# Optimization experiments

Measured on AMD Instinct MI355X. Metric: run time of the kernel, lower is better.

The kernel has to match this reference:

```python
import jax, jax.numpy as jnp
import numpy as np

N_NODES = 100000
N_EDGES = 1600000
N_FEAT = 512
N_HID = 256
N_CLASS = 40


def setup_inputs() -> dict:
    key = jax.random.key(0)
    ks = jax.random.split(key, 6)
    features = jax.random.normal(ks[0], (N_NODES, N_FEAT), dtype=jnp.float32)
    edge_index = jax.random.randint(ks[1], (2, N_EDGES), 0, N_NODES, dtype=jnp.int32)
    edge_weight = jax.random.uniform(ks[2], (N_EDGES,), dtype=jnp.float32)
    # xavier_uniform with gain=1.414 (as in reset_parameters)
    g = 1.414
    lim1 = g * np.sqrt(6.0 / (N_FEAT + N_HID))
    lim2 = g * np.sqrt(6.0 / (N_HID + N_CLASS))
    W1 = jax.random.uniform(ks[3], (N_FEAT, N_HID), minval=-lim1, maxval=lim1, dtype=jnp.float32)
    W2 = jax.random.uniform(ks[4], (N_HID, N_CLASS), minval=-lim2, maxval=lim2, dtype=jnp.float32)
    b1 = jnp.zeros((N_HID,), dtype=jnp.float32)
    b2 = jnp.zeros((N_CLASS,), dtype=jnp.float32)
    return {"features": features, "edge_index": edge_index, "edge_weight": edge_weight,
            "W1": W1, "b1": b1, "W2": W2, "b2": b2}


def _spmm(edge_index, edge_weight, x, n):
    # out[r] = sum over edges e with row[e]==r of w[e] * x[col[e]]
    row, col = edge_index[0], edge_index[1]
    msgs = edge_weight[:, None] * x[col]  # [E, D]
    return jax.ops.segment_sum(msgs, row, num_segments=n)


def reference(features, edge_index, edge_weight, W1, b1, W2, b2):
    n = features.shape[0]
    # Layer 1: linear -> spmm -> relu (dropout is identity in eval mode)
    h = features @ W1 + b1
    h = jax.nn.relu(_spmm(edge_index, edge_weight, h, n))
    # Layer 2: linear -> spmm -> log_softmax
    h = h @ W2 + b2
    h = _spmm(edge_index, edge_weight, h, n)
    return jax.nn.log_softmax(h, axis=1)
```

## Files before the change

### kernel.cpp

```cpp
#include <hip/hip_runtime.h>
#include <stdint.h>

#define N_NODES 100000
#define N_EDGES 1600000
#define N_FEAT 512
#define N_HID 256
#define N_CLASS 40
#define H2S 48

typedef float f32x4 __attribute__((ext_vector_type(4)));
typedef __bf16 bf16x8 __attribute__((ext_vector_type(8)));
typedef unsigned short u16x4 __attribute__((ext_vector_type(4)));
typedef unsigned short u16x8 __attribute__((ext_vector_type(8)));

__device__ __forceinline__ unsigned short f2bf(float f) {
  unsigned int u = __float_as_uint(f);
  unsigned int r = (u + 0x7FFFu + ((u >> 16) & 1u)) >> 16;
  return (unsigned short)r;
}
__device__ __forceinline__ float bf2f(unsigned short s) {
  return __uint_as_float(((unsigned int)s) << 16);
}

__device__ __forceinline__ void gll16(const void* g, void* l) {
  __builtin_amdgcn_global_load_lds(
      (const __attribute__((address_space(1))) unsigned int*)g,
      (__attribute__((address_space(3))) unsigned int*)l, 16, 0, 0);
}

#define HIST_BLOCKS 1563
#define W1T_BLOCKS  512
#define W2T_BLOCKS  48
__global__ __launch_bounds__(256) void k_pre(const float* __restrict__ W1,
                                             const float* __restrict__ W2,
                                             const int* __restrict__ ei,
                                             unsigned short* __restrict__ W1t,
                                             unsigned short* __restrict__ W2t,
                                             int* __restrict__ cnt,
                                             int* __restrict__ rank) {
  const int bid = blockIdx.x, tid = threadIdx.x;
  if (bid < HIST_BLOCKS) {
    #pragma unroll
    for (int k = 0; k < 4; ++k) {
      int e = bid * 1024 + k * 256 + tid;
      if (e < N_EDGES) rank[e] = atomicAdd(&cnt[ei[e]], 1);
    }
  } else if (bid < HIST_BLOCKS + W1T_BLOCKS) {
    int gid = (bid - HIST_BLOCKS) * 256 + tid;
    int n = gid >> 9, k = gid & 511;
    W1t[gid] = f2bf(W1[(long)k * N_HID + n]);
  } else {
    int gid = (bid - HIST_BLOCKS - W1T_BLOCKS) * 256 + tid;
    int n = gid >> 8, k = gid & 255;
    W2t[gid] = (n < N_CLASS) ? f2bf(W2[(long)k * N_CLASS + n]) : (unsigned short)0;
  }
}

__global__ __launch_bounds__(1024) void k_scan_a(const int* __restrict__ cnt,
                                                 int* __restrict__ rp,
                                                 int* __restrict__ bsum) {
  __shared__ int sm[1024];
  const int tid = threadIdx.x;
  const int i = blockIdx.x * 1024 + tid;
  int v = (i < N_NODES) ? cnt[i] : 0;
  sm[tid] = v;
  __syncthreads();
  #pragma unroll
  for (int d = 1; d < 1024; d <<= 1) {
    int t = (tid >= d) ? sm[tid - d] : 0;
    __syncthreads();
    sm[tid] += t;
    __syncthreads();
  }
  if (i < N_NODES) rp[i] = sm[tid] - v;
  if (tid == 1023) bsum[blockIdx.x] = sm[1023];
}

__global__ __launch_bounds__(128) void k_scan_b(const int* __restrict__ bsum,
                                                int* __restrict__ boffs,
                                                int* __restrict__ rp) {
  __shared__ int sm[128];
  const int tid = threadIdx.x;
  const int nb = (N_NODES + 1023) >> 10;
  int v = (tid < nb) ? bsum[tid] : 0;
  sm[tid] = v;
  __syncthreads();
  #pragma unroll
  for (int d = 1; d < 128; d <<= 1) {
    int t = (tid >= d) ? sm[tid - d] : 0;
    __syncthreads();
    sm[tid] += t;
    __syncthreads();
  }
  boffs[tid] = sm[tid] - v;
  if (tid == 127) rp[N_NODES] = sm[127];
}

__global__ void k_scan_c(int* __restrict__ rp, const int* __restrict__ boffs) {
  int i = blockIdx.x * 256 + threadIdx.x;
  if (i >= N_NODES) return;
  rp[i] += boffs[i >> 10];
}

#define NG1 782
__global__ __launch_bounds__(512) void k_fused1(const float* __restrict__ X,
                                                const unsigned short* __restrict__ W1t,
                                                const float* __restrict__ b1,
                                                unsigned short* __restrict__ H1,
                                                const int* __restrict__ ei,
                                                const float* __restrict__ ew,
                                                const int* __restrict__ rank,
                                                const int* __restrict__ rp,
                                                int2* __restrict__ cw) {
  const int t = threadIdx.x;

  if (blockIdx.x & 1) {
    int sb = blockIdx.x >> 1;
    #pragma unroll
    for (int k = 0; k < 4; ++k) {
      int e = sb * 2048 + k * 512 + t;
      if (e < N_EDGES) {
        int r = ei[e];
        int pos = rp[r] + rank[e];
        cw[pos] = make_int2(ei[N_EDGES + e], __float_as_int(ew[e]));
      }
    }
    return;
  }

  __shared__ __align__(16) float As[128 * 32];
  __shared__ __align__(16) unsigned short Bsm[256 * 32];
  const int gb = blockIdx.x >> 1;
  const long m0 = (long)gb * 128;
  const int lane = t & 63;
  const int wid = t >> 6;
  const int wm = wid >> 2, wn = wid & 3;
  const int lr = lane & 15;
  const int lkg = lane >> 4;

  const int a_row = t >> 3, a_ps = t & 7;
  const int b_row = t >> 2, b_ps = t & 3;
  long a_gr0 = m0 + a_row;      if (a_gr0 >= N_NODES) a_gr0 = N_NODES - 1;
  long a_gr1 = m0 + 64 + a_row; if (a_gr1 >= N_NODES) a_gr1 = N_NODES - 1;
  const float* a_src0 = X + a_gr0 * N_FEAT + ((a_ps ^ (a_row & 7)) << 2);
  const float* a_src1 = X + a_gr1 * N_FEAT + ((a_ps ^ (a_row & 7)) << 2);
  const unsigned short* b_src0 = W1t + (long)b_row * N_FEAT + ((b_ps ^ ((b_row >> 2) & 3)) << 3);
  const unsigned short* b_src1 = W1t + (long)(128 + b_row) * N_FEAT + ((b_ps ^ ((b_row >> 2) & 3)) << 3);
  char* a_dst = (char*)As + wid * 1024;
  char* b_dst = (char*)Bsm + wid * 1024;

  f32x4 acc[4][4] = {};

  for (int k0 = 0; k0 < N_FEAT; k0 += 32) {
    gll16(a_src0 + k0, a_dst);
    gll16(a_src1 + k0, a_dst + 8192);
    gll16(b_src0 + k0, b_dst);
    gll16(b_src1 + k0, b_dst + 8192);
    __syncthreads();

    bf16x8 bv[4];
    #pragma unroll
    for (int nt = 0; nt < 4; ++nt) {
      int row = wn * 64 + nt * 16 + lr;
      int ps = lkg ^ ((lr >> 2) & 3);
      bv[nt] = *(const bf16x8*)((const char*)Bsm + row * 64 + ps * 16);
    }
    #pragma unroll
    for (int mt = 0; mt < 4; ++mt) {
      int row = wm * 64 + mt * 16 + lr;
      int s0 = (2 * lkg) ^ (lr & 7);
      int s1 = (2 * lkg + 1) ^ (lr & 7);
      f32x4 xa = *(const f32x4*)((const char*)As + row * 128 + s0 * 16);
      f32x4 xb = *(const f32x4*)((const char*)As + row * 128 + s1 * 16);
      bf16x8 av;
      av[0] = (__bf16)xa[0]; av[1] = (__bf16)xa[1];
      av[2] = (__bf16)xa[2]; av[3] = (__bf16)xa[3];
      av[4] = (__bf16)xb[0]; av[5] = (__bf16)xb[1];
      av[6] = (__bf16)xb[2]; av[7] = (__bf16)xb[3];
      #pragma unroll
      for (int nt = 0; nt < 4; ++nt)
        acc[mt][nt] = __builtin_amdgcn_mfma_f32_16x16x32_bf16(av, bv[nt], acc[mt][nt], 0, 0, 0);
    }
    __syncthreads();
  }

  #pragma unroll
  for (int nt = 0; nt < 4; ++nt) {
    int col = wn * 64 + nt * 16 + lr;
    float bias = b1[col];
    #pragma unroll
    for (int mt = 0; mt < 4; ++mt) {
      #pragma unroll
      for (int i = 0; i < 4; ++i) {
        long row = m0 + wm * 64 + mt * 16 + lkg * 4 + i;
        if (row < N_NODES) H1[row * N_HID + col] = f2bf(acc[mt][nt][i] + bias);
      }
    }
  }
}

__global__ __launch_bounds__(256) void k_spmm1(const int* __restrict__ row_ptr,
                                               const int2* __restrict__ cw,
                                               const unsigned short* __restrict__ H1,
                                               unsigned short* __restrict__ H1r) {
  int r = blockIdx.x * 4 + (threadIdx.x >> 6);
  int lane = threadIdx.x & 63;
  if (r >= N_NODES) return;
  int s = row_ptr[r], e = row_ptr[r + 1];
  float a0 = 0.f, a1 = 0.f, a2 = 0.f, a3 = 0.f;
  const unsigned short* Hb = H1 + lane * 4;
  int i = s;
  for (; i + 8 <= e; i += 8) {
    int2 c0 = cw[i + 0]; int2 c1 = cw[i + 1]; int2 c2 = cw[i + 2]; int2 c3 = cw[i + 3];
    int2 c4 = cw[i + 4]; int2 c5 = cw[i + 5]; int2 c6 = cw[i + 6]; int2 c7 = cw[i + 7];
    u16x4 h0 = *(const u16x4*)(Hb + (long)c0.x * N_HID);
    u16x4 h1 = *(const u16x4*)(Hb + (long)c1.x * N_HID);
    u16x4 h2 = *(const u16x4*)(Hb + (long)c2.x * N_HID);
    u16x4 h3 = *(const u16x4*)(Hb + (long)c3.x * N_HID);
    u16x4 h4 = *(const u16x4*)(Hb + (long)c4.x * N_HID);
    u16x4 h5 = *(const u16x4*)(Hb + (long)c5.x * N_HID);
    u16x4 h6 = *(const u16x4*)(Hb + (long)c6.x * N_HID);
    u16x4 h7 = *(const u16x4*)(Hb + (long)c7.x * N_HID);
    float w0 = __int_as_float(c0.y), w1 = __int_as_float(c1.y);
    float w2 = __int_as_float(c2.y), w3 = __int_as_float(c3.y);
    float w4 = __int_as_float(c4.y), w5 = __int_as_float(c5.y);
    float w6 = __int_as_float(c6.y), w7 = __int_as_float(c7.y);
    a0 += w0 * bf2f(h0[0]); a1 += w0 * bf2f(h0[1]); a2 += w0 * bf2f(h0[2]); a3 += w0 * bf2f(h0[3]);
    a0 += w1 * bf2f(h1[0]); a1 += w1 * bf2f(h1[1]); a2 += w1 * bf2f(h1[2]); a3 += w1 * bf2f(h1[3]);
    a0 += w2 * bf2f(h2[0]); a1 += w2 * bf2f(h2[1]); a2 += w2 * bf2f(h2[2]); a3 += w2 * bf2f(h2[3]);
    a0 += w3 * bf2f(h3[0]); a1 += w3 * bf2f(h3[1]); a2 += w3 * bf2f(h3[2]); a3 += w3 * bf2f(h3[3]);
    a0 += w4 * bf2f(h4[0]); a1 += w4 * bf2f(h4[1]); a2 += w4 * bf2f(h4[2]); a3 += w4 * bf2f(h4[3]);
    a0 += w5 * bf2f(h5[0]); a1 += w5 * bf2f(h5[1]); a2 += w5 * bf2f(h5[2]); a3 += w5 * bf2f(h5[3]);
    a0 += w6 * bf2f(h6[0]); a1 += w6 * bf2f(h6[1]); a2 += w6 * bf2f(h6[2]); a3 += w6 * bf2f(h6[3]);
    a0 += w7 * bf2f(h7[0]); a1 += w7 * bf2f(h7[1]); a2 += w7 * bf2f(h7[2]); a3 += w7 * bf2f(h7[3]);
  }
  for (; i < e; ++i) {
    int2 cwv = cw[i];
    float w = __int_as_float(cwv.y);
    u16x4 hv = *(const u16x4*)(Hb + (long)cwv.x * N_HID);
    a0 += w * bf2f(hv[0]);
    a1 += w * bf2f(hv[1]);
    a2 += w * bf2f(hv[2]);
    a3 += w * bf2f(hv[3]);
  }
  u16x4 o;
  o[0] = f2bf(fmaxf(a0, 0.f));
  o[1] = f2bf(fmaxf(a1, 0.f));
  o[2] = f2bf(fmaxf(a2, 0.f));
  o[3] = f2bf(fmaxf(a3, 0.f));
  *(u16x4*)(H1r + (long)r * N_HID + lane * 4) = o;
}

__global__ __launch_bounds__(256) void k_gemm2(const unsigned short* __restrict__ H1r,
                                               const unsigned short* __restrict__ W2t,
                                               const float* __restrict__ b2,
                                               float* __restrict__ H2) {
  const int t = threadIdx.x;
  const int lane = t & 63;
  const int wid = t >> 6;
  const long m0 = (long)blockIdx.x * 128;
  const int lr = lane & 15;
  const int lk = (lane >> 4) * 8;

  const unsigned short* Ab[2];
  #pragma unroll
  for (int mt = 0; mt < 2; ++mt) {
    long r = m0 + wid * 32 + mt * 16 + lr;
    if (r >= N_NODES) r = N_NODES - 1;
    Ab[mt] = H1r + r * N_HID + lk;
  }
  const unsigned short* Bb[3];
  #pragma unroll
  for (int nt = 0; nt < 3; ++nt)
    Bb[nt] = W2t + (long)(nt * 16 + lr) * N_HID + lk;

  f32x4 acc[2][3] = {};
  #pragma unroll
  for (int k0 = 0; k0 < N_HID; k0 += 32) {
    bf16x8 av[2], bvv[3];
    #pragma unroll
    for (int mt = 0; mt < 2; ++mt) av[mt] = *(const bf16x8*)(Ab[mt] + k0);
    #pragma unroll
    for (int nt = 0; nt < 3; ++nt) bvv[nt] = *(const bf16x8*)(Bb[nt] + k0);
    #pragma unroll
    for (int mt = 0; mt < 2; ++mt)
      #pragma unroll
      for (int nt = 0; nt < 3; ++nt)
        acc[mt][nt] = __builtin_amdgcn_mfma_f32_16x16x32_bf16(av[mt], bvv[nt], acc[mt][nt], 0, 0, 0);
  }

  #pragma unroll
  for (int nt = 0; nt < 3; ++nt) {
    int col = nt * 16 + lr;
    if (col < N_CLASS) {
      float bias = b2[col];
      #pragma unroll
      for (int mt = 0; mt < 2; ++mt) {
        #pragma unroll
        for (int i = 0; i < 4; ++i) {
          long row = m0 + wid * 32 + mt * 16 + (lane >> 4) * 4 + i;
          if (row < N_NODES) H2[row * H2S + col] = acc[mt][nt][i] + bias;
        }
      }
    }
  }
}

__global__ __launch_bounds__(256) void k_spmm2_lsm(const int* __restrict__ row_ptr,
                                                   const int2* __restrict__ cw,
                                                   const float* __restrict__ H2,
                                                   float* __restrict__ out) {
  int r = blockIdx.x * 4 + (threadIdx.x >> 6);
  int lane = threadIdx.x & 63;
  if (r >= N_NODES) return;
  int s = row_ptr[r], e = row_ptr[r + 1];
  float acc = 0.f;
  const bool act = lane < N_CLASS;
  int i = s;
  for (; i + 8 <= e; i += 8) {
    int2 c0 = cw[i + 0]; int2 c1 = cw[i + 1]; int2 c2 = cw[i + 2]; int2 c3 = cw[i + 3];
    int2 c4 = cw[i + 4]; int2 c5 = cw[i + 5]; int2 c6 = cw[i + 6]; int2 c7 = cw[i + 7];
    float h0 = 0.f, h1 = 0.f, h2 = 0.f, h3 = 0.f, h4 = 0.f, h5 = 0.f, h6 = 0.f, h7 = 0.f;
    if (act) {
      h0 = H2[(long)c0.x * H2S + lane];
      h1 = H2[(long)c1.x * H2S + lane];
      h2 = H2[(long)c2.x * H2S + lane];
      h3 = H2[(long)c3.x * H2S + lane];
      h4 = H2[(long)c4.x * H2S + lane];
      h5 = H2[(long)c5.x * H2S + lane];
      h6 = H2[(long)c6.x * H2S + lane];
      h7 = H2[(long)c7.x * H2S + lane];
    }
    acc += __int_as_float(c0.y) * h0;
    acc += __int_as_float(c1.y) * h1;
    acc += __int_as_float(c2.y) * h2;
    acc += __int_as_float(c3.y) * h3;
    acc += __int_as_float(c4.y) * h4;
    acc += __int_as_float(c5.y) * h5;
    acc += __int_as_float(c6.y) * h6;
    acc += __int_as_float(c7.y) * h7;
  }
  for (; i < e; ++i) {
    int2 cwv = cw[i];
    if (act) acc += __int_as_float(cwv.y) * H2[(long)cwv.x * H2S + lane];
  }
  float v = act ? acc : -INFINITY;
  float m = v;
  #pragma unroll
  for (int d = 32; d > 0; d >>= 1) m = fmaxf(m, __shfl_xor(m, d));
  float ex = act ? __expf(v - m) : 0.f;
  float ssum = ex;
  #pragma unroll
  for (int d = 32; d > 0; d >>= 1) ssum += __shfl_xor(ssum, d);
  float ls = __logf(ssum);
  if (act) out[(long)r * N_CLASS + lane] = v - m - ls;
}

extern "C" void kernel_launch(void* const* d_in, const int* in_sizes, int n_in,
                              void* d_out, int out_size, void* d_ws, size_t ws_size,
                              hipStream_t stream) {
  (void)in_sizes; (void)n_in; (void)out_size; (void)ws_size;
  const float* X  = (const float*)d_in[0];
  const int*   EI = (const int*)d_in[1];
  const float* EW = (const float*)d_in[2];
  const float* W1 = (const float*)d_in[3];
  const float* b1 = (const float*)d_in[4];
  const float* W2 = (const float*)d_in[5];
  const float* b2 = (const float*)d_in[6];
  float* out = (float*)d_out;

  char* p = (char*)d_ws;
  auto take = [&](size_t bytes) {
    char* r = p;
    p += (bytes + 511) & ~(size_t)511;
    return r;
  };
  unsigned short* W1t   = (unsigned short*)take((size_t)N_HID * N_FEAT * 2);
  unsigned short* W2t   = (unsigned short*)take((size_t)48 * N_HID * 2);
  int*            cnt   = (int*)take((size_t)N_NODES * 4);
  int*            rp    = (int*)take((size_t)(N_NODES + 1) * 4);
  int*            bsum  = (int*)take((size_t)128 * 4);
  int*            boffs = (int*)take((size_t)128 * 4);
  int*            rank  = (int*)take((size_t)N_EDGES * 4);
  int2*           cw    = (int2*)take((size_t)N_EDGES * 8);
  unsigned short* H1    = (unsigned short*)take((size_t)N_NODES * N_HID * 2);
  unsigned short* H1r   = (unsigned short*)take((size_t)N_NODES * N_HID * 2);
  float*          H2    = (float*)take((size_t)N_NODES * H2S * 4);

  const int NB_SCAN = (N_NODES + 1023) / 1024;

  hipMemsetAsync(cnt, 0, (size_t)N_NODES * 4, stream);
  k_pre<<<HIST_BLOCKS + W1T_BLOCKS + W2T_BLOCKS, 256, 0, stream>>>(W1, W2, EI, W1t, W2t, cnt, rank);
  k_scan_a<<<NB_SCAN, 1024, 0, stream>>>(cnt, rp, bsum);
  k_scan_b<<<1, 128, 0, stream>>>(bsum, boffs, rp);
  k_scan_c<<<(N_NODES + 255) / 256, 256, 0, stream>>>(rp, boffs);
  k_fused1<<<2 * NG1, 512, 0, stream>>>(X, W1t, b1, H1, EI, EW, rank, rp, cw);
  k_spmm1<<<(N_NODES + 3) / 4, 256, 0, stream>>>(rp, cw, H1, H1r);
  k_gemm2<<<(N_NODES + 127) / 128, 256, 0, stream>>>(H1r, W2t, b2, H2);
  k_spmm2_lsm<<<(N_NODES + 3) / 4, 256, 0, stream>>>(rp, cw, H2, out);
}
```

Measured before the change: 461.4 us.

## Pack CSR column and bf16 weight into one word; restructure GEMM1 with resident W1 panel

Edge entries are packed into a single 32-bit word (17-bit column index, 15-bit truncated bf16 weight), halving CSR traffic in both SpMM passes and allowing uint4 vector loads. The fused GEMM+scatter kernel is split into a separate scatter kernel and a new GEMM1 that keeps a 128-column W1 panel entirely in LDS (128 KB), with each wave streaming X rows directly from global memory rather than staging them through LDS. This removes the per-k-step barriers, but it sacrifices the overlap between the scatter and the GEMM, reduces edge-weight precision to 15 bits, and limits the GEMM to 250 blocks.

Result: faster. 427.0 us (-7.5%).

```diff
diff --git a/kernel.cpp b/kernel.cpp
--- a/kernel.cpp
+++ b/kernel.cpp
@@ -21,12 +21,10 @@
 __device__ __forceinline__ float bf2f(unsigned short s) {
   return __uint_as_float(((unsigned int)s) << 16);
 }
-
-__device__ __forceinline__ void gll16(const void* g, void* l) {
-  __builtin_amdgcn_global_load_lds(
-      (const __attribute__((address_space(1))) unsigned int*)g,
-      (__attribute__((address_space(3))) unsigned int*)l, 16, 0, 0);
-}
+__device__ __forceinline__ float pk_w(unsigned int p) {
+  return __uint_as_float((p >> 17) << 16);
+}
+__device__ __forceinline__ int pk_c(unsigned int p) { return (int)(p & 0x1FFFFu); }
 
 #define HIST_BLOCKS 1563
 #define W1T_BLOCKS  512
@@ -102,105 +100,89 @@
   rp[i] += boffs[i >> 10];
 }
 
-#define NG1 782
-__global__ __launch_bounds__(512) void k_fused1(const float* __restrict__ X,
+__global__ __launch_bounds__(512) void k_scatter(const int* __restrict__ ei,
+                                                 const float* __restrict__ ew,
+                                                 const int* __restrict__ rank,
+                                                 const int* __restrict__ rp,
+                                                 unsigned int* __restrict__ cwp) {
+  const int t = threadIdx.x;
+  #pragma unroll
+  for (int k = 0; k < 4; ++k) {
+    int e = blockIdx.x * 2048 + k * 512 + t;
+    if (e < N_EDGES) {
+      int r = ei[e];
+      int pos = rp[r] + rank[e];
+      unsigned int w15 = (unsigned int)f2bf(ew[e]);
+      cwp[pos] = (w15 << 17) | (unsigned int)ei[N_EDGES + e];
+    }
+  }
+}
+
+__global__ __launch_bounds__(1024) void k_gemm1(const float* __restrict__ X,
                                                 const unsigned short* __restrict__ W1t,
                                                 const float* __restrict__ b1,
-                                                unsigned short* __restrict__ H1,
-                                                const int* __restrict__ ei,
-                                                const float* __restrict__ ew,
-                                                const int* __restrict__ rank,
-                                                const int* __restrict__ rp,
-                                                int2* __restrict__ cw) {
+                                                unsigned short* __restrict__ H1) {
+  __shared__ __align__(16) unsigned short Bs[128 * 512];
   const int t = threadIdx.x;
-
-  if (blockIdx.x & 1) {
-    int sb = blockIdx.x >> 1;
-    #pragma unroll
-    for (int k = 0; k < 4; ++k) {
-      int e = sb * 2048 + k * 512 + t;
-      if (e < N_EDGES) {
-        int r = ei[e];
-        int pos = rp[r] + rank[e];
-        cw[pos] = make_int2(ei[N_EDGES + e], __float_as_int(ew[e]));
-      }
-    }
-    return;
-  }
-
-  __shared__ __align__(16) float As[128 * 32];
-  __shared__ __align__(16) unsigned short Bsm[256 * 32];
-  const int gb = blockIdx.x >> 1;
-  const long m0 = (long)gb * 128;
+  const int pair = blockIdx.x >> 1, panel = blockIdx.x & 1;
+  const long rb = (long)pair * 800;
+  const int n0 = panel * 128;
+
+  {
+    const int col = t >> 3, seg = t & 7;
+    const unsigned short* src = W1t + (long)(n0 + col) * N_FEAT;
+    #pragma unroll
+    for (int j = 0; j < 8; ++j) {
+      int slot = seg * 8 + j;
+      int ps = slot ^ (col & 7);
+      *(u16x8*)&Bs[col * 512 + ps * 8] = *(const u16x8*)(src + slot * 8);
+    }
+  }
+  __syncthreads();
+
   const int lane = t & 63;
   const int wid = t >> 6;
-  const int wm = wid >> 2, wn = wid & 3;
   const int lr = lane & 15;
   const int lkg = lane >> 4;
 
-  const int a_row = t >> 3, a_ps = t & 7;
-  const int b_row = t >> 2, b_ps = t & 3;
-  long a_gr0 = m0 + a_row;      if (a_gr0 >= N_NODES) a_gr0 = N_NODES - 1;
-  long a_gr1 = m0 + 64 + a_row; if (a_gr1 >= N_NODES) a_gr1 = N_NODES - 1;
-  const float* a_src0 = X + a_gr0 * N_FEAT + ((a_ps ^ (a_row & 7)) << 2);
-  const float* a_src1 = X + a_gr1 * N_FEAT + ((a_ps ^ (a_row & 7)) << 2);
-  const unsigned short* b_src0 = W1t + (long)b_row * N_FEAT + ((b_ps ^ ((b_row >> 2) & 3)) << 3);
-  const unsigned short* b_src1 = W1t + (long)(128 + b_row) * N_FEAT + ((b_ps ^ ((b_row >> 2) & 3)) << 3);
-  char* a_dst = (char*)As + wid * 1024;
-  char* b_dst = (char*)Bsm + wid * 1024;
-
-  f32x4 acc[4][4] = {};
-
-  for (int k0 = 0; k0 < N_FEAT; k0 += 32) {
-    gll16(a_src0 + k0, a_dst);
-    gll16(a_src1 + k0, a_dst + 8192);
-    gll16(b_src0 + k0, b_dst);
-    gll16(b_src1 + k0, b_dst + 8192);
-    __syncthreads();
-
-    bf16x8 bv[4];
-    #pragma unroll
-    for (int nt = 0; nt < 4; ++nt) {
-      int row = wn * 64 + nt * 16 + lr;
-      int ps = lkg ^ ((lr >> 2) & 3);
-      bv[nt] = *(const bf16x8*)((const char*)Bsm + row * 64 + ps * 16);
-    }
-    #pragma unroll
-    for (int mt = 0; mt < 4; ++mt) {
-      int row = wm * 64 + mt * 16 + lr;
-      int s0 = (2 * lkg) ^ (lr & 7);
-      int s1 = (2 * lkg + 1) ^ (lr & 7);
-      f32x4 xa = *(const f32x4*)((const char*)As + row * 128 + s0 * 16);
-      f32x4 xb = *(const f32x4*)((const char*)As + row * 128 + s1 * 16);
+  for (int c = wid; c < 50; c += 16) {
+    const long row0 = rb + c * 16;
+    const float* ap = X + (row0 + lr) * N_FEAT + lkg * 8;
+    f32x4 acc[8] = {};
+
+    #pragma unroll 2
+    for (int k0 = 0; k0 < N_FEAT; k0 += 32) {
+      f32x4 xa = *(const f32x4*)(ap + k0);
+      f32x4 xb = *(const f32x4*)(ap + k0 + 4);
       bf16x8 av;
       av[0] = (__bf16)xa[0]; av[1] = (__bf16)xa[1];
       av[2] = (__bf16)xa[2]; av[3] = (__bf16)xa[3];
       av[4] = (__bf16)xb[0]; av[5] = (__bf16)xb[1];
       av[6] = (__bf16)xb[2]; av[7] = (__bf16)xb[3];
+      const int slot = (k0 >> 3) + lkg;
+      const int ps = slot ^ (lr & 7);
       #pragma unroll
-      for (int nt = 0; nt < 4; ++nt)
-        acc[mt][nt] = __builtin_amdgcn_mfma_f32_16x16x32_bf16(av, bv[nt], acc[mt][nt], 0, 0, 0);
-    }
-    __syncthreads();
-  }
-
-  #pragma unroll
-  for (int nt = 0; nt < 4; ++nt) {
-    int col = wn * 64 + nt * 16 + lr;
-    float bias = b1[col];
-    #pragma unroll
-    for (int mt = 0; mt < 4; ++mt) {
+      for (int nt = 0; nt < 8; ++nt) {
+        bf16x8 bv = *(const bf16x8*)&Bs[(nt * 16 + lr) * 512 + ps * 8];
+        acc[nt] = __builtin_amdgcn_mfma_f32_16x16x32_bf16(av, bv, acc[nt], 0, 0, 0);
+      }
+    }
+
+    #pragma unroll
+    for (int nt = 0; nt < 8; ++nt) {
+      int colg = n0 + nt * 16 + lr;
+      float bias = b1[colg];
       #pragma unroll
       for (int i = 0; i < 4; ++i) {
-        long row = m0 + wm * 64 + mt * 16 + lkg * 4 + i;
-        if (row < N_NODES) H1[row * N_HID + col] = f2bf(acc[mt][nt][i] + bias);
+        long row = row0 + lkg * 4 + i;
+        H1[row * N_HID + colg] = f2bf(acc[nt][i] + bias);
       }
     }
   }
 }
 
 __global__ __launch_bounds__(256) void k_spmm1(const int* __restrict__ row_ptr,
-                                               const int2* __restrict__ cw,
+                                               const unsigned int* __restrict__ cwp,
                                                const unsigned short* __restrict__ H1,
                                                unsigned short* __restrict__ H1r) {
   int r = blockIdx.x * 4 + (threadIdx.x >> 6);
@@ -211,20 +193,18 @@
   const unsigned short* Hb = H1 + lane * 4;
   int i = s;
   for (; i + 8 <= e; i += 8) {
-    int2 c0 = cw[i + 0]; int2 c1 = cw[i + 1]; int2 c2 = cw[i + 2]; int2 c3 = cw[i + 3];
-    int2 c4 = cw[i + 4]; int2 c5 = cw[i + 5]; int2 c6 = cw[i + 6]; int2 c7 = cw[i + 7];
-    u16x4 h0 = *(const u16x4*)(Hb + (long)c0.x * N_HID);
-    u16x4 h1 = *(const u16x4*)(Hb + (long)c1.x * N_HID);
-    u16x4 h2 = *(const u16x4*)(Hb + (long)c2.x * N_HID);
-    u16x4 h3 = *(const u16x4*)(Hb + (long)c3.x * N_HID);
-    u16x4 h4 = *(const u16x4*)(Hb + (long)c4.x * N_HID);
-    u16x4 h5 = *(const u16x4*)(Hb + (long)c5.x * N_HID);
-    u16x4 h6 = *(const u16x4*)(Hb + (long)c6.x * N_HID);
-    u16x4 h7 = *(const u16x4*)(Hb + (long)c7.x * N_HID);
-    float w0 = __int_as_float(c0.y), w1 = __int_as_float(c1.y);
-    float w2 = __int_as_float(c2.y), w3 = __int_as_float(c3.y);
-    float w4 = __int_as_float(c4.y), w5 = __int_as_float(c5.y);
-    float w6 = __int_as_float(c6.y), w7 = __int_as_float(c7.y);
+    uint4 ca = *(const uint4*)(cwp + i);
+    uint4 cb = *(const uint4*)(cwp + i + 4);
+    u16x4 h0 = *(const u16x4*)(Hb + (long)pk_c(ca.x) * N_HID);
+    u16x4 h1 = *(const u16x4*)(Hb + (long)pk_c(ca.y) * N_HID);
+    u16x4 h2 = *(const u16x4*)(Hb + (long)pk_c(ca.z) * N_HID);
+    u16x4 h3 = *(const u16x4*)(Hb + (long)pk_c(ca.w) * N_HID);
+    u16x4 h4 = *(const u16x4*)(Hb + (long)pk_c(cb.x) * N_HID);
+    u16x4 h5 = *(const u16x4*)(Hb + (long)pk_c(cb.y) * N_HID);
+    u16x4 h6 = *(const u16x4*)(Hb + (long)pk_c(cb.z) * N_HID);
+    u16x4 h7 = *(const u16x4*)(Hb + (long)pk_c(cb.w) * N_HID);
+    float w0 = pk_w(ca.x), w1 = pk_w(ca.y), w2 = pk_w(ca.z), w3 = pk_w(ca.w);
+    float w4 = pk_w(cb.x), w5 = pk_w(cb.y), w6 = pk_w(cb.z), w7 = pk_w(cb.w);
     a0 += w0 * bf2f(h0[0]); a1 += w0 * bf2f(h0[1]); a2 += w0 * bf2f(h0[2]); a3 += w0 * bf2f(h0[3]);
     a0 += w1 * bf2f(h1[0]); a1 += w1 * bf2f(h1[1]); a2 += w1 * bf2f(h1[2]); a3 += w1 * bf2f(h1[3]);
     a0 += w2 * bf2f(h2[0]); a1 += w2 * bf2f(h2[1]); a2 += w2 * bf2f(h2[2]); a3 += w2 * bf2f(h2[3]);
@@ -235,9 +215,9 @@
     a0 += w7 * bf2f(h7[0]); a1 += w7 * bf2f(h7[1]); a2 += w7 * bf2f(h7[2]); a3 += w7 * bf2f(h7[3]);
   }
   for (; i < e; ++i) {
-    int2 cwv = cw[i];
-    float w = __int_as_float(cwv.y);
-    u16x4 hv = *(const u16x4*)(Hb + (long)cwv.x * N_HID);
+    unsigned int p = cwp[i];
+    float w = pk_w(p);
+    u16x4 hv = *(const u16x4*)(Hb + (long)pk_c(p) * N_HID);
     a0 += w * bf2f(hv[0]);
     a1 += w * bf2f(hv[1]);
     a2 += w * bf2f(hv[2]);
@@ -307,7 +287,7 @@
 }
 
 __global__ __launch_bounds__(256) void k_spmm2_lsm(const int* __restrict__ row_ptr,
-                                                   const int2* __restrict__ cw,
+                                                   const unsigned int* __restrict__ cwp,
                                                    const float* __restrict__ H2,
                                                    float* __restrict__ out) {
   int r = blockIdx.x * 4 + (threadIdx.x >> 6);
@@ -318,31 +298,31 @@
   const bool act = lane < N_CLASS;
   int i = s;
   for (; i + 8 <= e; i += 8) {
-    int2 c0 = cw[i + 0]; int2 c1 = cw[i + 1]; int2 c2 = cw[i + 2]; int2 c3 = cw[i + 3];
-    int2 c4 = cw[i + 4]; int2 c5 = cw[i + 5]; int2 c6 = cw[i + 6]; int2 c7 = cw[i + 7];
+    uint4 ca = *(const uint4*)(cwp + i);
+    uint4 cb = *(const uint4*)(cwp + i + 4);
     float h0 = 0.f, h1 = 0.f, h2 = 0.f, h3 = 0.f, h4 = 0.f, h5 = 0.f, h6 = 0.f, h7 = 0.f;
     if (act) {
-      h0 = H2[(long)c0.x * H2S + lane];
-      h1 = H2[(long)c1.x * H2S + lane];
-      h2 = H2[(long)c2.x * H2S + lane];
-      h3 = H2[(long)c3.x * H2S + lane];
-      h4 = H2[(long)c4.x * H2S + lane];
-      h5 = H2[(long)c5.x * H2S + lane];
-      h6 = H2[(long)c6.x * H2S + lane];
-      h7 = H2[(long)c7.x * H2S + lane];
-    }
-    acc += __int_as_float(c0.y) * h0;
-    acc += __int_as_float(c1.y) * h1;
-    acc += __int_as_float(c2.y) * h2;
-    acc += __int_as_float(c3.y) * h3;
-    acc += __int_as_float(c4.y) * h4;
-    acc += __int_as_float(c5.y) * h5;
-    acc += __int_as_float(c6.y) * h6;
-    acc += __int_as_float(c7.y) * h7;
+      h0 = H2[(long)pk_c(ca.x) * H2S + lane];
+      h1 = H2[(long)pk_c(ca.y) * H2S + lane];
+      h2 = H2[(long)pk_c(ca.z) * H2S + lane];
+      h3 = H2[(long)pk_c(ca.w) * H2S + lane];
+      h4 = H2[(long)pk_c(cb.x) * H2S + lane];
+      h5 = H2[(long)pk_c(cb.y) * H2S + lane];
+      h6 = H2[(long)pk_c(cb.z) * H2S + lane];
+      h7 = H2[(long)pk_c(cb.w) * H2S + lane];
+    }
+    acc += pk_w(ca.x) * h0;
+    acc += pk_w(ca.y) * h1;
+    acc += pk_w(ca.z) * h2;
+    acc += pk_w(ca.w) * h3;
+    acc += pk_w(cb.x) * h4;
+    acc += pk_w(cb.y) * h5;
+    acc += pk_w(cb.z) * h6;
+    acc += pk_w(cb.w) * h7;
   }
   for (; i < e; ++i) {
-    int2 cwv = cw[i];
-    if (act) acc += __int_as_float(cwv.y) * H2[(long)cwv.x * H2S + lane];
+    unsigned int p = cwp[i];
+    if (act) acc += pk_w(p) * H2[(long)pk_c(p) * H2S + lane];
   }
   float v = act ? acc : -INFINITY;
   float m = v;
@@ -382,7 +362,7 @@
   int*            bsum  = (int*)take((size_t)128 * 4);
   int*            boffs = (int*)take((size_t)128 * 4);
   int*            rank  = (int*)take((size_t)N_EDGES * 4);
-  int2*           cw    = (int2*)take((size_t)N_EDGES * 8);
+  unsigned int*   cwp   = (unsigned int*)take((size_t)N_EDGES * 4);
   unsigned short* H1    = (unsigned short*)take((size_t)N_NODES * N_HID * 2);
   unsigned short* H1r   = (unsigned short*)take((size_t)N_NODES * N_HID * 2);
   float*          H2    = (float*)take((size_t)N_NODES * H2S * 4);
@@ -394,8 +374,9 @@
   k_scan_a<<<NB_SCAN, 1024, 0, stream>>>(cnt, rp, bsum);
   k_scan_b<<<1, 128, 0, stream>>>(bsum, boffs, rp);
   k_scan_c<<<(N_NODES + 255) / 256, 256, 0, stream>>>(rp, boffs);
-  k_fused1<<<2 * NG1, 512, 0, stream>>>(X, W1t, b1, H1, EI, EW, rank, rp, cw);
-  k_spmm1<<<(N_NODES + 3) / 4, 256, 0, stream>>>(rp, cw, H1, H1r);
+  k_scatter<<<(N_EDGES + 2047) / 2048, 512, 0, stream>>>(EI, EW, rank, rp, cwp);
+  k_gemm1<<<250, 1024, 0, stream>>>(X, W1t, b1, H1);
+  k_spmm1<<<(N_NODES + 3) / 4, 256, 0, stream>>>(rp, cwp, H1, H1r);
   k_gemm2<<<(N_NODES + 127) / 128, 256, 0, stream>>>(H1r, W2t, b2, H2);
-  k_spmm2_lsm<<<(N_NODES + 3) / 4, 256, 0, stream>>>(rp, cw, H2, out);
-}
+  k_spmm2_lsm<<<(N_NODES + 3) / 4, 256, 0, stream>>>(rp, cwp, H2, out);
+}
```
